# Kernel tuning notes

Measured on AMD Instinct MI355X. Metric: run time of the kernel, lower is better.

The kernel has to match this reference:

```python
import jax, jax.numpy as jnp
import numpy as np

B, S, D, H, DFF = 4, 2048, 1024, 16, 4096
DK = D // H
EPS = 1e-9


def setup_inputs() -> dict:
    key = jax.random.key(0)
    ks = jax.random.split(key, 12)
    s = lambda k, shape, scale: jax.random.normal(k, shape, dtype=jnp.float32) * scale
    return {
        "x": s(ks[0], (B, S, D), 1.0),
        "mask": jnp.ones((B, 1, 1, S), dtype=jnp.int32),
        # Linear weights stored torch-style [out, in]
        "wq": s(ks[1], (D, D), D ** -0.5),
        "wk": s(ks[2], (D, D), D ** -0.5),
        "wv": s(ks[3], (D, D), D ** -0.5),
        "wo": s(ks[4], (D, D), D ** -0.5),
        "w1": s(ks[5], (DFF, D), D ** -0.5),
        "b1": jnp.zeros((DFF,), jnp.float32),
        "w2": s(ks[6], (D, DFF), DFF ** -0.5),
        "b2": jnp.zeros((D,), jnp.float32),
        "g1": jnp.ones((D,), jnp.float32),
        "be1": jnp.zeros((D,), jnp.float32),
        "g2": jnp.ones((D,), jnp.float32),
        "be2": jnp.zeros((D,), jnp.float32),
    }


def _layernorm(x, gamma, beta):
    # Matches AddAndNorm: torch.std uses Bessel correction (ddof=1)
    mean = jnp.mean(x, axis=-1, keepdims=True)
    var = jnp.sum((x - mean) ** 2, axis=-1, keepdims=True) / (x.shape[-1] - 1)
    return gamma * (x - mean) / jnp.sqrt(var + EPS) + beta


def _mha(x, mask, wq, wk, wv, wo):
    b, s, d = x.shape
    def proj(w):  # [b,s,d] @ [d,d]^T -> heads [b,h,s,dk]
        return (x @ w.T).reshape(b, s, H, DK).transpose(0, 2, 1, 3)
    q, k, v = proj(wq), proj(wk), proj(wv)
    scores = jnp.einsum("bhqd,bhkd->bhqk", q, k) / jnp.sqrt(jnp.float32(DK))
    scores = jnp.where(mask == 0, jnp.float32(-1e9), scores)
    attn = jax.nn.softmax(scores, axis=-1)
    out = jnp.einsum("bhqk,bhkd->bhqd", attn, v)
    out = out.transpose(0, 2, 1, 3).reshape(b, s, d)
    return out @ wo.T


def reference(x, mask, wq, wk, wv, wo, w1, b1, w2, b2, g1, be1, g2, be2):
    # Residual 1: x + MHA(LN(x))  (dropout = 0)
    h1 = x + _mha(_layernorm(x, g1, be1), mask, wq, wk, wv, wo)
    # Residual 2: h1 + FFN(LN(h1))
    z = _layernorm(h1, g2, be2)
    ffn = jax.nn.relu(z @ w1.T + b1) @ w2.T + b2
    return h1 + ffn
```

## Files before the change

kernel.cpp:

```cpp
#include <hip/hip_runtime.h>
#include <hip/hip_bf16.h>
#include <cstdint>
#include <cstddef>

typedef __attribute__((ext_vector_type(8))) short short8;
typedef __attribute__((ext_vector_type(4))) float floatx4;
typedef __attribute__((ext_vector_type(4))) unsigned short ushort4e;

#define B_   4
#define S_   2048
#define D_   1024
#define H_   16
#define DK_  64
#define DFF_ 4096
#define MTOT (B_ * S_)

__device__ __forceinline__ float bf2f(unsigned short u) {
    union { unsigned int i; float f; } v; v.i = ((unsigned int)u) << 16; return v.f;
}
__device__ __forceinline__ unsigned short f2bf(float f) {
    union { float f; unsigned int i; } v; v.f = f;
    unsigned int u = v.i;
    u += 0x7fffu + ((u >> 16) & 1u);
    return (unsigned short)(u >> 16);
}
__device__ __forceinline__ unsigned int pkbf(float a, float b) {
    union { float f; unsigned int u; } x, y; x.f = a; y.f = b;
    return ((x.u + 0x8000u) >> 16) | ((y.u + 0x8000u) & 0xffff0000u);
}
__device__ __forceinline__ void async_cp16(const void* g, void* l) {
    __builtin_amdgcn_global_load_lds(
        (const __attribute__((address_space(1))) unsigned int*)g,
        (__attribute__((address_space(3))) unsigned int*)l,
        16, 0, 0);
}

__global__ void dtype_probe(const unsigned short* __restrict__ x, int* flag) {
    __shared__ float red[4];
    const int tid = threadIdx.x;
    float mx = 0.f;
    #pragma unroll
    for (int i = 0; i < 16; i++) {
        float v = fabsf(bf2f(x[tid * 16 + i]));
        if (v != v) v = 1e30f;
        mx = fmaxf(mx, v);
    }
    #pragma unroll
    for (int off = 32; off > 0; off >>= 1) mx = fmaxf(mx, __shfl_down(mx, off));
    if ((tid & 63) == 0) red[tid >> 6] = mx;
    __syncthreads();
    if (tid == 0) {
        float m = fmaxf(fmaxf(red[0], red[1]), fmaxf(red[2], red[3]));
        *flag = (m > 50.f) ? 1 : 0;
    }
}

__device__ __forceinline__ void cvt8(const void* src, unsigned short* dst, int i, int fl) {
    if (fl) {
        const floatx4* s = (const floatx4*)src;
        floatx4 a = s[i * 2], b = s[i * 2 + 1];
        short8 o;
        o[0] = (short)f2bf(a[0]); o[1] = (short)f2bf(a[1]);
        o[2] = (short)f2bf(a[2]); o[3] = (short)f2bf(a[3]);
        o[4] = (short)f2bf(b[0]); o[5] = (short)f2bf(b[1]);
        o[6] = (short)f2bf(b[2]); o[7] = (short)f2bf(b[3]);
        ((short8*)dst)[i] = o;
    } else {
        ((short8*)dst)[i] = ((const short8*)src)[i];
    }
}

__global__ void cvt_kernel(const void* __restrict__ src,
                           unsigned short* __restrict__ dst,
                           int n8, const int* __restrict__ flag) {
    const int i = blockIdx.x * 256 + threadIdx.x;
    if (i >= n8) return;
    cvt8(src, dst, i, *flag);
}

__global__ void cvt4_kernel(const void* s0, const void* s1, const void* s2, const void* s3,
                            unsigned short* __restrict__ dst,
                            const int* __restrict__ flag) {
    const int t = blockIdx.x >> 9;
    const int i = (blockIdx.x & 511) * 256 + threadIdx.x;
    const void* s = (t == 0) ? s0 : (t == 1) ? s1 : (t == 2) ? s2 : s3;
    cvt8(s, dst + (size_t)t * (D_ * D_), i, *flag);
}

__global__ void cvt_small(const void* b1, const void* b2, const void* g1,
                          const void* be1, const void* g2, const void* be2,
                          unsigned short* db1, unsigned short* db2, unsigned short* dg1,
                          unsigned short* dbe1, unsigned short* dg2, unsigned short* dbe2,
                          const int* __restrict__ flag) {
    const int fl = *flag;
    for (int i = threadIdx.x; i < 1152; i += 256) {
        if (i < 512)       cvt8(b1,  db1,  i,        fl);
        else if (i < 640)  cvt8(b2,  db2,  i - 512,  fl);
        else if (i < 768)  cvt8(g1,  dg1,  i - 640,  fl);
        else if (i < 896)  cvt8(be1, dbe1, i - 768,  fl);
        else if (i < 1024) cvt8(g2,  dg2,  i - 896,  fl);
        else               cvt8(be2, dbe2, i - 1024, fl);
    }
}

#define BM 128
#define BN 128
#define BK 64

template<int RELU, int HAS_BIAS, int RES_MODE, int OUT_MODE>
__global__ __launch_bounds__(256)
void gemm_bt(const unsigned short* __restrict__ A, int lda,
             const unsigned short* __restrict__ W, int ldw,
             const unsigned short* __restrict__ bias,
             const void* resid,
             void* out,
             int M, int N, int K,
             const int* __restrict__ flagp)
{
    __shared__ unsigned short As[BM * BK];
    __shared__ unsigned short Bs[BN * BK];

    const int tid  = threadIdx.x;
    const int lane = tid & 63;
    const int wave = tid >> 6;
    const int wm = wave >> 1;
    const int wn = wave & 1;
    const int lr = lane & 15;
    const int lq = lane >> 4;

    const int m0 = blockIdx.y * BM;
    const int n0 = blockIdx.x * BN;

    int fl = 1;
    if (RES_MODE == 3 || OUT_MODE == 2) fl = *flagp;

    floatx4 acc[4][4];
    #pragma unroll
    for (int i = 0; i < 4; i++)
        #pragma unroll
        for (int j = 0; j < 4; j++)
            acc[i][j] = (floatx4){0.f, 0.f, 0.f, 0.f};

    const int lrow = lane >> 3;
    const int lcol = (lane & 7) * 8;

    for (int k0 = 0; k0 < K; k0 += BK) {
        #pragma unroll
        for (int t = 0; t < 4; t++) {
            const int row = wave * 32 + t * 8;
            async_cp16(A + (size_t)(m0 + row + lrow) * lda + k0 + lcol, &As[row * BK]);
            async_cp16(W + (size_t)(n0 + row + lrow) * ldw + k0 + lcol, &Bs[row * BK]);
        }
        __syncthreads();
        #pragma unroll
        for (int kk = 0; kk < BK; kk += 32) {
            short8 af[4], bfr[4];
            #pragma unroll
            for (int i = 0; i < 4; i++) {
                af[i]  = *(const short8*)(&As[(wm * 64 + i * 16 + lr) * BK + kk + lq * 8]);
                bfr[i] = *(const short8*)(&Bs[(wn * 64 + i * 16 + lr) * BK + kk + lq * 8]);
            }
            #pragma unroll
            for (int i = 0; i < 4; i++)
                #pragma unroll
                for (int j = 0; j < 4; j++)
                    acc[i][j] = __builtin_amdgcn_mfma_f32_16x16x32_bf16(
                                    af[i], bfr[j], acc[i][j], 0, 0, 0);
        }
        __syncthreads();
    }

    #pragma unroll
    for (int i = 0; i < 4; i++) {
        #pragma unroll
        for (int j = 0; j < 4; j++) {
            const int col = n0 + wn * 64 + j * 16 + lr;
            const float bv = HAS_BIAS ? bf2f(bias[col]) : 0.f;
            #pragma unroll
            for (int r = 0; r < 4; r++) {
                const int row = m0 + wm * 64 + i * 16 + lq * 4 + r;
                const size_t idx = (size_t)row * N + col;
                float vvv = acc[i][j][r] + bv;
                if (RES_MODE == 1) vvv += bf2f(((const unsigned short*)resid)[idx]);
                if (RES_MODE == 2) vvv += ((const float*)resid)[idx];
                if (RES_MODE == 3) vvv += fl ? ((const float*)resid)[idx]
                                             : bf2f(((const unsigned short*)resid)[idx]);
                if (RELU) vvv = fmaxf(vvv, 0.f);
                if (OUT_MODE == 1)      ((float*)out)[idx] = vvv;
                else if (OUT_MODE == 0) ((unsigned short*)out)[idx] = f2bf(vvv);
                else { if (fl) ((float*)out)[idx] = vvv;
                       else    ((unsigned short*)out)[idx] = f2bf(vvv); }
            }
        }
    }
}

template<int IN_MODE>
__global__ __launch_bounds__(256)
void ln_kernel(const void* __restrict__ Xv,
               const unsigned short* __restrict__ g,
               const unsigned short* __restrict__ be,
               unsigned short* __restrict__ out,
               const int* __restrict__ flagp)
{
    const int row = blockIdx.x;
    const int tid = threadIdx.x;
    int fl = 1;
    if (IN_MODE == 2) fl = *flagp;
    float x4[4];
    if (IN_MODE == 1 || fl) {
        const float* X = (const float*)Xv + (size_t)row * D_ + tid * 4;
        floatx4 t = *(const floatx4*)X;
        x4[0] = t[0]; x4[1] = t[1]; x4[2] = t[2]; x4[3] = t[3];
    } else {
        const unsigned short* X = (const unsigned short*)Xv + (size_t)row * D_ + tid * 4;
        ushort4e u = *(const ushort4e*)X;
        #pragma unroll
        for (int i = 0; i < 4; i++) x4[i] = bf2f(u[i]);
    }
    float s1 = x4[0] + x4[1] + x4[2] + x4[3];
    float s2 = x4[0]*x4[0] + x4[1]*x4[1] + x4[2]*x4[2] + x4[3]*x4[3];
    #pragma unroll
    for (int off = 32; off > 0; off >>= 1) {
        s1 += __shfl_down(s1, off);
        s2 += __shfl_down(s2, off);
    }
    __shared__ float r1[4], r2[4];
    const int wv = tid >> 6;
    if ((tid & 63) == 0) { r1[wv] = s1; r2[wv] = s2; }
    __syncthreads();
    s1 = r1[0] + r1[1] + r1[2] + r1[3];
    s2 = r2[0] + r2[1] + r2[2] + r2[3];
    const float mean = s1 * (1.0f / D_);
    const float var  = (s2 - (float)D_ * mean * mean) * (1.0f / (D_ - 1));
    const float rstd = rsqrtf(var + 1e-9f);

    ushort4e o4;
    #pragma unroll
    for (int i = 0; i < 4; i++) {
        const float gv = bf2f(g[tid * 4 + i]);
        const float bv = bf2f(be[tid * 4 + i]);
        o4[i] = f2bf(gv * (x4[i] - mean) * rstd + bv);
    }
    *(ushort4e*)(out + (size_t)row * D_ + tid * 4) = o4;
}

__global__ __launch_bounds__(256)
void vtrans(const unsigned short* __restrict__ V, unsigned short* __restrict__ Vt)
{
    __shared__ unsigned short t[64 * 72];
    const int tid = threadIdx.x;
    const int kt  = blockIdx.x * 64;
    const int bh  = blockIdx.y;
    const int b   = bh >> 4, h = bh & 15;
    const int r   = tid >> 2;
    const int c4  = (tid & 3) * 16;
    const unsigned short* vp = V + (size_t)(b * S_ + kt + r) * D_ + h * DK_ + c4;
    *(short8*)&t[r * 72 + c4]     = *(const short8*)vp;
    *(short8*)&t[r * 72 + c4 + 8] = *(const short8*)(vp + 8);
    __syncthreads();
    short8 o0, o1;
    #pragma unroll
    for (int e = 0; e < 8; e++) {
        o0[e] = (short)t[(c4 + e) * 72 + r];
        o1[e] = (short)t[(c4 + 8 + e) * 72 + r];
    }
    unsigned short* op = Vt + ((size_t)bh * DK_ + r) * S_ + kt + c4;
    *(short8*)op       = o0;
    *(short8*)(op + 8) = o1;
}

#define ATK 64
#define KLD 72

__global__ __launch_bounds__(256)
void attn_mfma(const unsigned short* __restrict__ Q,
               const unsigned short* __restrict__ Kg,
               const unsigned short* __restrict__ Vt,
               const int* __restrict__ mask,
               unsigned short* __restrict__ ctx)
{
    __shared__ unsigned short Ks[ATK * KLD];
    __shared__ unsigned short Vts[DK_ * KLD];
    __shared__ unsigned short Ps[4][32 * KLD];
    __shared__ float maskadd[ATK];
    __shared__ float ared[4][32];

    const int tid  = threadIdx.x;
    const int lane = tid & 63;
    const int w    = tid >> 6;
    const int c    = lane & 15;
    const int qd   = lane >> 4;
    const int bh   = blockIdx.y;
    const int b    = bh >> 4;
    const int h    = bh & 15;
    const int q0   = blockIdx.x * 128 + w * 32;

    const float QS = 0.18033688f;
    short8 qf[2][2];
    #pragma unroll
    for (int jq = 0; jq < 2; jq++)
        #pragma unroll
        for (int kk = 0; kk < 2; kk++) {
            const unsigned short* qp =
                Q + (size_t)(b * S_ + q0 + jq * 16 + c) * D_ + h * DK_ + kk * 32 + qd * 8;
            short8 t = *(const short8*)qp;
            short8 o;
            #pragma unroll
            for (int e = 0; e < 8; e++)
                o[e] = (short)f2bf(bf2f((unsigned short)t[e]) * QS);
            qf[jq][kk] = o;
        }

    floatx4 acc_o[2][4];
    #pragma unroll
    for (int iq = 0; iq < 2; iq++)
        #pragma unroll
        for (int jd = 0; jd < 4; jd++)
            acc_o[iq][jd] = (floatx4){0.f, 0.f, 0.f, 0.f};
    float lrun[2] = {0.f, 0.f};

    const int srow = tid >> 2;
    const int scol = (tid & 3) * 16;

    for (int kt = 0; kt < S_; kt += ATK) {
        {
            const unsigned short* kp = Kg + (size_t)(b * S_ + kt + srow) * D_ + h * DK_ + scol;
            *(short8*)&Ks[srow * KLD + scol]     = *(const short8*)kp;
            *(short8*)&Ks[srow * KLD + scol + 8] = *(const short8*)(kp + 8);
            const unsigned short* vp = Vt + ((size_t)bh * DK_ + srow) * S_ + kt + scol;
            *(short8*)&Vts[srow * KLD + scol]     = *(const short8*)vp;
            *(short8*)&Vts[srow * KLD + scol + 8] = *(const short8*)(vp + 8);
            if (tid < ATK) maskadd[tid] = (mask[b * S_ + kt + tid] == 0) ? -1e9f : 0.f;
        }
        __syncthreads();

        floatx4 acc_s[4][2];
        #pragma unroll
        for (int i = 0; i < 4; i++)
            #pragma unroll
            for (int jq = 0; jq < 2; jq++)
                acc_s[i][jq] = (floatx4){0.f, 0.f, 0.f, 0.f};
        #pragma unroll
        for (int kk = 0; kk < 2; kk++) {
            short8 kf[4];
            #pragma unroll
            for (int i = 0; i < 4; i++)
                kf[i] = *(const short8*)&Ks[(i * 16 + c) * KLD + kk * 32 + qd * 8];
            #pragma unroll
            for (int i = 0; i < 4; i++)
                #pragma unroll
                for (int jq = 0; jq < 2; jq++)
                    acc_s[i][jq] = __builtin_amdgcn_mfma_f32_16x16x32_bf16(
                                       kf[i], qf[jq][kk], acc_s[i][jq], 0, 0, 0);
        }

        floatx4 madd[4];
        #pragma unroll
        for (int i = 0; i < 4; i++)
            madd[i] = *(const floatx4*)&maskadd[i * 16 + qd * 4];

        #pragma unroll
        for (int jq = 0; jq < 2; jq++) {
            float ps = 0.f;
            #pragma unroll
            for (int i = 0; i < 4; i++) {
                #pragma unroll
                for (int r = 0; r < 4; r++) {
                    float p = __builtin_amdgcn_exp2f(acc_s[i][jq][r] + madd[i][r]);
                    acc_s[i][jq][r] = p;
                    ps += p;
                }
                uint2 pk;
                pk.x = pkbf(acc_s[i][jq][0], acc_s[i][jq][1]);
                pk.y = pkbf(acc_s[i][jq][2], acc_s[i][jq][3]);
                *(uint2*)&Ps[w][(jq * 16 + c) * KLD + i * 16 + qd * 4] = pk;
            }
            ps += __shfl_xor(ps, 16);
            ps += __shfl_xor(ps, 32);
            lrun[jq] += ps;
        }

        #pragma unroll
        for (int kk = 0; kk < 2; kk++) {
            short8 pf[2], vf[4];
            #pragma unroll
            for (int iq = 0; iq < 2; iq++)
                pf[iq] = *(const short8*)&Ps[w][(iq * 16 + c) * KLD + kk * 32 + qd * 8];
            #pragma unroll
            for (int jd = 0; jd < 4; jd++)
                vf[jd] = *(const short8*)&Vts[(jd * 16 + c) * KLD + kk * 32 + qd * 8];
            #pragma unroll
            for (int iq = 0; iq < 2; iq++)
                #pragma unroll
                for (int jd = 0; jd < 4; jd++)
                    acc_o[iq][jd] = __builtin_amdgcn_mfma_f32_16x16x32_bf16(
                                        pf[iq], vf[jd], acc_o[iq][jd], 0, 0, 0);
        }
        __syncthreads();
    }

    if (lane < 16) { ared[w][c] = 1.f / lrun[0]; ared[w][16 + c] = 1.f / lrun[1]; }
    floatx4 lv0 = *(const floatx4*)&ared[w][qd * 4];
    floatx4 lv1 = *(const floatx4*)&ared[w][16 + qd * 4];
    #pragma unroll
    for (int iq = 0; iq < 2; iq++)
        #pragma unroll
        for (int jd = 0; jd < 4; jd++)
            #pragma unroll
            for (int r = 0; r < 4; r++) {
                const int row = q0 + iq * 16 + qd * 4 + r;
                const int col = h * DK_ + jd * 16 + c;
                const float inv = (iq == 0) ? lv0[r] : lv1[r];
                ctx[(size_t)(b * S_ + row) * D_ + col] = f2bf(acc_o[iq][jd][r] * inv);
            }
}

extern "C" void kernel_launch(void* const* d_in, const int* in_sizes, int n_in,
                              void* d_out, int out_size, void* d_ws, size_t ws_size,
                              hipStream_t stream)
{
    const void* x_raw  = d_in[0];
    const int*  mask   = (const int*)d_in[1];
    const void* wq_raw = d_in[2];
    const void* wk_raw = d_in[3];
    const void* wv_raw = d_in[4];
    const void* wo_raw = d_in[5];
    const void* w1_raw = d_in[6];
    const void* b1_raw = d_in[7];
    const void* w2_raw = d_in[8];
    const void* b2_raw = d_in[9];
    const void* g1_raw = d_in[10];
    const void* be1_raw= d_in[11];
    const void* g2_raw = d_in[12];
    const void* be2_raw= d_in[13];

    char* ws = (char*)d_ws;
    const size_t MB = 1024 * 1024;
    int* flag = (int*)ws;
    unsigned short* cb1  = (unsigned short*)(ws + 1 * 1024);
    unsigned short* cb2  = (unsigned short*)(ws + 16 * 1024);
    unsigned short* cg1  = (unsigned short*)(ws + 32 * 1024);
    unsigned short* cbe1 = (unsigned short*)(ws + 40 * 1024);
    unsigned short* cg2  = (unsigned short*)(ws + 48 * 1024);
    unsigned short* cbe2 = (unsigned short*)(ws + 56 * 1024);
    unsigned short* cwqkvo = (unsigned short*)(ws + 1 * MB);
    unsigned short* cwq  = cwqkvo;
    unsigned short* cwk  = cwqkvo + 1 * (D_ * D_);
    unsigned short* cwv  = cwqkvo + 2 * (D_ * D_);
    unsigned short* cwo  = cwqkvo + 3 * (D_ * D_);
    unsigned short* cw1  = (unsigned short*)(ws + 9 * MB);
    unsigned short* cw2  = (unsigned short*)(ws + 17 * MB);
    unsigned short* xn1  = (unsigned short*)(ws + 25 * MB);
    unsigned short* zbuf = (unsigned short*)(ws + 25 * MB);
    unsigned short* vt   = (unsigned short*)(ws + 41 * MB);
    unsigned short* q    = (unsigned short*)(ws + 57 * MB);
    unsigned short* k    = (unsigned short*)(ws + 73 * MB);
    float*          h1   = (float*)(ws + 57 * MB);
    unsigned short* v    = (unsigned short*)d_out;
    unsigned short* ctx  = (unsigned short*)d_out;
    unsigned short* xn2  = (unsigned short*)d_out;

    dtype_probe<<<1, 256, 0, stream>>>((const unsigned short*)x_raw, flag);
    cvt_small<<<1, 256, 0, stream>>>(b1_raw, b2_raw, g1_raw, be1_raw, g2_raw, be2_raw,
                                     cb1, cb2, cg1, cbe1, cg2, cbe2, flag);
    cvt4_kernel<<<2048, 256, 0, stream>>>(wq_raw, wk_raw, wv_raw, wo_raw, cwqkvo, flag);
    cvt_kernel<<<(DFF_ * D_ / 8 + 255) / 256, 256, 0, stream>>>(w1_raw, cw1, DFF_ * D_ / 8, flag);
    cvt_kernel<<<(D_ * DFF_ / 8 + 255) / 256, 256, 0, stream>>>(w2_raw, cw2, D_ * DFF_ / 8, flag);

    const dim3 blk(256);
    const dim3 gs(D_ / BN, MTOT / BM);
    const dim3 gs2(2048 / BN, MTOT / BM);

    ln_kernel<2><<<MTOT, blk, 0, stream>>>(x_raw, cg1, cbe1, xn1, flag);
    gemm_bt<0,0,0,0><<<gs, blk, 0, stream>>>(xn1, D_, cwq, D_, nullptr, nullptr, q, MTOT, D_, D_, flag);
    gemm_bt<0,0,0,0><<<gs, blk, 0, stream>>>(xn1, D_, cwk, D_, nullptr, nullptr, k, MTOT, D_, D_, flag);
    gemm_bt<0,0,0,0><<<gs, blk, 0, stream>>>(xn1, D_, cwv, D_, nullptr, nullptr, v, MTOT, D_, D_, flag);
    vtrans<<<dim3(S_ / 64, B_ * H_), blk, 0, stream>>>(v, vt);
    attn_mfma<<<dim3(S_ / 128, B_ * H_), blk, 0, stream>>>(q, k, vt, mask, ctx);
    gemm_bt<0,0,3,1><<<gs, blk, 0, stream>>>(ctx, D_, cwo, D_, nullptr, x_raw, h1, MTOT, D_, D_, flag);
    ln_kernel<1><<<MTOT, blk, 0, stream>>>(h1, cg2, cbe2, xn2, flag);
    {
        gemm_bt<1,1,0,0><<<gs2, blk, 0, stream>>>(xn2, D_, cw1, D_, cb1, nullptr, zbuf, MTOT, 2048, D_, flag);
        gemm_bt<0,0,2,1><<<gs, blk, 0, stream>>>(zbuf, 2048, cw2, DFF_, nullptr, h1, h1, MTOT, D_, 2048, flag);
        const unsigned short* w1c = cw1 + (size_t)2048 * D_;
        gemm_bt<1,1,0,0><<<gs2, blk, 0, stream>>>(xn2, D_, w1c, D_, cb1 + 2048, nullptr, zbuf, MTOT, 2048, D_, flag);
        gemm_bt<0,1,2,2><<<gs, blk, 0, stream>>>(zbuf, 2048, cw2 + 2048, DFF_, cb2, h1, d_out, MTOT, D_, 2048, flag);
    }
}
```

Measured before the change: 652.6 us.

## Fuse QKV projections into one GEMM and async-load K/V tiles in attention

Replaces the three separate Q, K and V projection GEMMs with a single GEMM over the concatenated weight into an interleaved QKV buffer with row stride 3072. The attention kernel now reads Q and K from that buffer and stages K and V^T tiles into LDS with direct global-to-LDS async copies, using an unpadded 64-wide LDS layout. This cuts launch count and repeated reads of the normalized input and frees registers on the staging path. In exchange the unpadded LDS layout may raise bank conflicts on fragment reads, and the workspace buffers are reshuffled (ctx now aliases xn1/zbuf, vt lives in the output).

```diff
diff --git a/kernel.cpp b/kernel.cpp
--- a/kernel.cpp
+++ b/kernel.cpp
@@ -14,6 +14,7 @@
 #define DK_  64
 #define DFF_ 4096
 #define MTOT (B_ * S_)
+#define QKVLD 3072
 
 __device__ __forceinline__ float bf2f(unsigned short u) {
     union { unsigned int i; float f; } v; v.i = ((unsigned int)u) << 16; return v.f;
@@ -246,7 +247,8 @@
 }
 
 __global__ __launch_bounds__(256)
-void vtrans(const unsigned short* __restrict__ V, unsigned short* __restrict__ Vt)
+void vtrans(const unsigned short* __restrict__ V, int ldv,
+            unsigned short* __restrict__ Vt)
 {
     __shared__ unsigned short t[64 * 72];
     const int tid = threadIdx.x;
@@ -255,7 +257,7 @@
     const int b   = bh >> 4, h = bh & 15;
     const int r   = tid >> 2;
     const int c4  = (tid & 3) * 16;
-    const unsigned short* vp = V + (size_t)(b * S_ + kt + r) * D_ + h * DK_ + c4;
+    const unsigned short* vp = V + (size_t)(b * S_ + kt + r) * ldv + h * DK_ + c4;
     *(short8*)&t[r * 72 + c4]     = *(const short8*)vp;
     *(short8*)&t[r * 72 + c4 + 8] = *(const short8*)(vp + 8);
     __syncthreads();
@@ -270,19 +272,19 @@
     *(short8*)(op + 8) = o1;
 }
 
-#define ATK 64
-#define KLD 72
+#define ATK   64
+#define KS_LD 64
+#define PS_LD 72
 
 __global__ __launch_bounds__(256)
-void attn_mfma(const unsigned short* __restrict__ Q,
-               const unsigned short* __restrict__ Kg,
+void attn_mfma(const unsigned short* __restrict__ QKV,
                const unsigned short* __restrict__ Vt,
                const int* __restrict__ mask,
                unsigned short* __restrict__ ctx)
 {
-    __shared__ unsigned short Ks[ATK * KLD];
-    __shared__ unsigned short Vts[DK_ * KLD];
-    __shared__ unsigned short Ps[4][32 * KLD];
+    __shared__ unsigned short Ks[ATK * KS_LD];
+    __shared__ unsigned short Vts[DK_ * KS_LD];
+    __shared__ unsigned short Ps[4][32 * PS_LD];
     __shared__ float maskadd[ATK];
     __shared__ float ared[4][32];
 
@@ -296,6 +298,9 @@
     const int h    = bh & 15;
     const int q0   = blockIdx.x * 128 + w * 32;
 
+    const int lrow = lane >> 3;
+    const int lcol = (lane & 7) * 8;
+
     const float QS = 0.18033688f;
     short8 qf[2][2];
     #pragma unroll
@@ -303,7 +308,7 @@
         #pragma unroll
         for (int kk = 0; kk < 2; kk++) {
             const unsigned short* qp =
-                Q + (size_t)(b * S_ + q0 + jq * 16 + c) * D_ + h * DK_ + kk * 32 + qd * 8;
+                QKV + (size_t)(b * S_ + q0 + jq * 16 + c) * QKVLD + h * DK_ + kk * 32 + qd * 8;
             short8 t = *(const short8*)qp;
             short8 o;
             #pragma unroll
@@ -320,17 +325,19 @@
             acc_o[iq][jd] = (floatx4){0.f, 0.f, 0.f, 0.f};
     float lrun[2] = {0.f, 0.f};
 
-    const int srow = tid >> 2;
-    const int scol = (tid & 3) * 16;
-
     for (int kt = 0; kt < S_; kt += ATK) {
         {
-            const unsigned short* kp = Kg + (size_t)(b * S_ + kt + srow) * D_ + h * DK_ + scol;
-            *(short8*)&Ks[srow * KLD + scol]     = *(const short8*)kp;
-            *(short8*)&Ks[srow * KLD + scol + 8] = *(const short8*)(kp + 8);
-            const unsigned short* vp = Vt + ((size_t)bh * DK_ + srow) * S_ + kt + scol;
-            *(short8*)&Vts[srow * KLD + scol]     = *(const short8*)vp;
-            *(short8*)&Vts[srow * KLD + scol + 8] = *(const short8*)(vp + 8);
+            const unsigned short* kbase =
+                QKV + 1024 + (size_t)(b * S_ + kt + w * 16) * QKVLD + h * DK_;
+            const unsigned short* vbase =
+                Vt + ((size_t)bh * DK_ + w * 16) * S_ + kt;
+            #pragma unroll
+            for (int t = 0; t < 2; t++) {
+                async_cp16(kbase + (size_t)(t * 8 + lrow) * QKVLD + lcol,
+                           &Ks[(w * 16 + t * 8) * KS_LD]);
+                async_cp16(vbase + (size_t)(t * 8 + lrow) * S_ + lcol,
+                           &Vts[(w * 16 + t * 8) * KS_LD]);
+            }
             if (tid < ATK) maskadd[tid] = (mask[b * S_ + kt + tid] == 0) ? -1e9f : 0.f;
         }
         __syncthreads();
@@ -346,7 +353,7 @@
             short8 kf[4];
             #pragma unroll
             for (int i = 0; i < 4; i++)
-                kf[i] = *(const short8*)&Ks[(i * 16 + c) * KLD + kk * 32 + qd * 8];
+                kf[i] = *(const short8*)&Ks[(i * 16 + c) * KS_LD + kk * 32 + qd * 8];
             #pragma unroll
             for (int i = 0; i < 4; i++)
                 #pragma unroll
@@ -374,7 +381,7 @@
                 uint2 pk;
                 pk.x = pkbf(acc_s[i][jq][0], acc_s[i][jq][1]);
                 pk.y = pkbf(acc_s[i][jq][2], acc_s[i][jq][3]);
-                *(uint2*)&Ps[w][(jq * 16 + c) * KLD + i * 16 + qd * 4] = pk;
+                *(uint2*)&Ps[w][(jq * 16 + c) * PS_LD + i * 16 + qd * 4] = pk;
             }
             ps += __shfl_xor(ps, 16);
             ps += __shfl_xor(ps, 32);
@@ -386,10 +393,10 @@
             short8 pf[2], vf[4];
             #pragma unroll
             for (int iq = 0; iq < 2; iq++)
-                pf[iq] = *(const short8*)&Ps[w][(iq * 16 + c) * KLD + kk * 32 + qd * 8];
+                pf[iq] = *(const short8*)&Ps[w][(iq * 16 + c) * PS_LD + kk * 32 + qd * 8];
             #pragma unroll
             for (int jd = 0; jd < 4; jd++)
-                vf[jd] = *(const short8*)&Vts[(jd * 16 + c) * KLD + kk * 32 + qd * 8];
+                vf[jd] = *(const short8*)&Vts[(jd * 16 + c) * KS_LD + kk * 32 + qd * 8];
             #pragma unroll
             for (int iq = 0; iq < 2; iq++)
                 #pragma unroll
@@ -445,20 +452,16 @@
     unsigned short* cg2  = (unsigned short*)(ws + 48 * 1024);
     unsigned short* cbe2 = (unsigned short*)(ws + 56 * 1024);
     unsigned short* cwqkvo = (unsigned short*)(ws + 1 * MB);
-    unsigned short* cwq  = cwqkvo;
-    unsigned short* cwk  = cwqkvo + 1 * (D_ * D_);
-    unsigned short* cwv  = cwqkvo + 2 * (D_ * D_);
-    unsigned short* cwo  = cwqkvo + 3 * (D_ * D_);
+    unsigned short* cwqkv  = cwqkvo;
+    unsigned short* cwo    = cwqkvo + 3 * (D_ * D_);
     unsigned short* cw1  = (unsigned short*)(ws + 9 * MB);
     unsigned short* cw2  = (unsigned short*)(ws + 17 * MB);
     unsigned short* xn1  = (unsigned short*)(ws + 25 * MB);
+    unsigned short* ctx  = (unsigned short*)(ws + 25 * MB);
     unsigned short* zbuf = (unsigned short*)(ws + 25 * MB);
-    unsigned short* vt   = (unsigned short*)(ws + 41 * MB);
-    unsigned short* q    = (unsigned short*)(ws + 57 * MB);
-    unsigned short* k    = (unsigned short*)(ws + 73 * MB);
+    unsigned short* qkv  = (unsigned short*)(ws + 41 * MB);
     float*          h1   = (float*)(ws + 57 * MB);
-    unsigned short* v    = (unsigned short*)d_out;
-    unsigned short* ctx  = (unsigned short*)d_out;
+    unsigned short* vt   = (unsigned short*)d_out;
     unsigned short* xn2  = (unsigned short*)d_out;
 
     dtype_probe<<<1, 256, 0, stream>>>((const unsigned short*)x_raw, flag);
@@ -470,21 +473,18 @@
 
     const dim3 blk(256);
     const dim3 gs(D_ / BN, MTOT / BM);
+    const dim3 gsq(QKVLD / BN, MTOT / BM);
     const dim3 gs2(2048 / BN, MTOT / BM);
 
     ln_kernel<2><<<MTOT, blk, 0, stream>>>(x_raw, cg1, cbe1, xn1, flag);
-    gemm_bt<0,0,0,0><<<gs, blk, 0, stream>>>(xn1, D_, cwq, D_, nullptr, nullptr, q, MTOT, D_, D_, flag);
-    gemm_bt<0,0,0,0><<<gs, blk, 0, stream>>>(xn1, D_, cwk, D_, nullptr, nullptr, k, MTOT, D_, D_, flag);
-    gemm_bt<0,0,0,0><<<gs, blk, 0, stream>>>(xn1, D_, cwv, D_, nullptr, nullptr, v, MTOT, D_, D_, flag);
-    vtrans<<<dim3(S_ / 64, B_ * H_), blk, 0, stream>>>(v, vt);
-    attn_mfma<<<dim3(S_ / 128, B_ * H_), blk, 0, stream>>>(q, k, vt, mask, ctx);
+    gemm_bt<0,0,0,0><<<gsq, blk, 0, stream>>>(xn1, D_, cwqkv, D_, nullptr, nullptr, qkv, MTOT, QKVLD, D_, flag);
+    vtrans<<<dim3(S_ / 64, B_ * H_), blk, 0, stream>>>(qkv + 2048, QKVLD, vt);
+    attn_mfma<<<dim3(S_ / 128, B_ * H_), blk, 0, stream>>>(qkv, vt, mask, ctx);
     gemm_bt<0,0,3,1><<<gs, blk, 0, stream>>>(ctx, D_, cwo, D_, nullptr, x_raw, h1, MTOT, D_, D_, flag);
     ln_kernel<1><<<MTOT, blk, 0, stream>>>(h1, cg2, cbe2, xn2, flag);
-    {
-        gemm_bt<1,1,0,0><<<gs2, blk, 0, stream>>>(xn2, D_, cw1, D_, cb1, nullptr, zbuf, MTOT, 2048, D_, flag);
-        gemm_bt<0,0,2,1><<<gs, blk, 0, stream>>>(zbuf, 2048, cw2, DFF_, nullptr, h1, h1, MTOT, D_, 2048, flag);
-        const unsigned short* w1c = cw1 + (size_t)2048 * D_;
-        gemm_bt<1,1,0,0><<<gs2, blk, 0, stream>>>(xn2, D_, w1c, D_, cb1 + 2048, nullptr, zbuf, MTOT, 2048, D_, flag);
-        gemm_bt<0,1,2,2><<<gs, blk, 0, stream>>>(zbuf, 2048, cw2 + 2048, DFF_, cb2, h1, d_out, MTOT, D_, 2048, flag);
-    }
-}
+    gemm_bt<1,1,0,0><<<gs2, blk, 0, stream>>>(xn2, D_, cw1, D_, cb1, nullptr, zbuf, MTOT, 2048, D_, flag);
+    gemm_bt<0,0,2,1><<<gs, blk, 0, stream>>>(zbuf, 2048, cw2, DFF_, nullptr, h1, h1, MTOT, D_, 2048, flag);
+    const unsigned short* w1c = cw1 + (size_t)2048 * D_;
+    gemm_bt<1,1,0,0><<<gs2, blk, 0, stream>>>(xn2, D_, w1c, D_, cb1 + 2048, nullptr, zbuf, MTOT, 2048, D_, flag);
+    gemm_bt<0,1,2,2><<<gs, blk, 0, stream>>>(zbuf, 2048, cw2 + 2048, DFF_, cb2, h1, d_out, MTOT, D_, 2048, flag);
+}
```

Measured after the change: 649.9 us. No clear change (-0.4%).
